# Kernel tuning notes

Measured on AMD Instinct MI355X. Metric: run time of the kernel, lower is better.

Reference implementation:

```python
import jax, jax.numpy as jnp
import numpy as np

DIM = 384
HEADS = 12
WS = 7
HID = 4 * 256  # FFN hidden is hard-coded default 1024, NOT 4*dim
EPS = 1e-5


def layernorm(x, g, b):
    mu = jnp.mean(x, axis=-1, keepdims=True)
    var = jnp.mean(jnp.square(x - mu), axis=-1, keepdims=True)
    return (x - mu) * jax.lax.rsqrt(var + EPS) * g + b


def setup_inputs() -> dict:
    key = jax.random.key(0)
    ks = jax.random.split(key, 12)
    s = 0.02
    return {
        "x": jax.random.normal(ks[0], (32, DIM, 56, 56), dtype=jnp.float32),
        "ln1_g": jnp.ones((DIM,), jnp.float32),
        "ln1_b": jnp.zeros((DIM,), jnp.float32),
        "qkv_w": jax.random.normal(ks[1], (3 * DIM, DIM), jnp.float32) * s,
        "qkv_b": jnp.zeros((3 * DIM,), jnp.float32),
        "proj_w": jax.random.normal(ks[2], (DIM, DIM), jnp.float32) * s,
        "proj_b": jnp.zeros((DIM,), jnp.float32),
        "ln2_g": jnp.ones((DIM,), jnp.float32),
        "ln2_b": jnp.zeros((DIM,), jnp.float32),
        "fc1_w": jax.random.normal(ks[3], (HID, DIM), jnp.float32) * s,
        "fc1_b": jnp.zeros((HID,), jnp.float32),
        "fc2_w": jax.random.normal(ks[4], (DIM, HID), jnp.float32) * s,
        "fc2_b": jnp.zeros((DIM,), jnp.float32),
    }


def window_attention(x, qkv_w, qkv_b, proj_w, proj_b):
    # x: [B, H, W, C] channels-last
    B, H, W, C = x.shape
    Wh, Ww = H // WS, W // WS
    # partition: [B*Wh*Ww, WS*WS, C]
    w = x.reshape(B, Wh, WS, Ww, WS, C).transpose(0, 1, 3, 2, 4, 5)
    w = w.reshape(B * Wh * Ww, WS * WS, C)
    Bn, N, _ = w.shape
    hd = C // HEADS
    qkv = w @ qkv_w.T + qkv_b  # [Bn, N, 3C]
    qkv = qkv.reshape(Bn, N, 3, HEADS, hd).transpose(2, 0, 3, 1, 4)
    q, k, v = qkv[0], qkv[1], qkv[2]  # each [Bn, h, N, hd]
    attn = jnp.einsum('bhnd,bhmd->bhnm', q, k) * (hd ** -0.5)
    attn = jax.nn.softmax(attn, axis=-1)
    o = jnp.einsum('bhnm,bhmd->bhnd', attn, v)
    o = o.transpose(0, 2, 1, 3).reshape(Bn, N, C)
    o = o @ proj_w.T + proj_b
    # reverse
    o = o.reshape(B, Wh, Ww, WS, WS, C).transpose(0, 1, 3, 2, 4, 5)
    return o.reshape(B, H, W, C)


def reference(x, ln1_g, ln1_b, qkv_w, qkv_b, proj_w, proj_b,
              ln2_g, ln2_b, fc1_w, fc1_b, fc2_w, fc2_b):
    # x: [B, C, H, W]
    residual = x
    h = x.transpose(0, 2, 3, 1)  # [B,H,W,C]
    h = layernorm(h, ln1_g, ln1_b)
    h = window_attention(h, qkv_w, qkv_b, proj_w, proj_b)
    x = h.transpose(0, 3, 1, 2) + residual
    residual = x
    h = x.transpose(0, 2, 3, 1)
    h = layernorm(h, ln2_g, ln2_b)
    h = jax.nn.gelu(h @ fc1_w.T + fc1_b, approximate=False)
    h = h @ fc2_w.T + fc2_b
    return h.transpose(0, 3, 1, 2) + residual
```

## Files before the change

### kernel.cpp

```cpp
#include <hip/hip_runtime.h>
#include <cstdint>
#include <cmath>

#define DIM 384
#define HEADS 12
#define TOKENS 100352
#define HW_ 3136
#define NWIN 2048

typedef __attribute__((ext_vector_type(8))) short short8;
typedef __attribute__((ext_vector_type(4))) short short4v;
typedef __attribute__((ext_vector_type(2))) short short2v;
typedef __attribute__((ext_vector_type(4))) float f32x4;

#define AS1 __attribute__((address_space(1)))
#define AS3 __attribute__((address_space(3)))

__device__ __forceinline__ short f2b(float f){
  unsigned u = __builtin_bit_cast(unsigned, f);
  u += 0x7FFFu + ((u >> 16) & 1u);
  return (short)(u >> 16);
}
__device__ __forceinline__ float b2f(short h){
  unsigned u = ((unsigned)(unsigned short)h) << 16;
  return __builtin_bit_cast(float, u);
}

__device__ __forceinline__ void gload_lds16(const short* g, short* l){
  __builtin_amdgcn_global_load_lds((AS1 void*)(g), (AS3 void*)(l), 16, 0, 0);
}

__device__ __forceinline__ float gelu_f(float v){
  float z  = v * 0.70710678118654752f;
  float az = fabsf(z);
  float t  = __builtin_amdgcn_rcpf(1.f + 0.3275911f*az);
  float poly = t*(0.254829592f + t*(-0.284496736f + t*(1.421413741f +
               t*(-1.453152027f + t*1.061405429f))));
  float e  = __expf(-z*z);
  float er = copysignf(1.f - poly*e, z);
  return 0.5f * v * (1.f + er);
}

__global__ void k_cvt(const float* __restrict__ s, short* __restrict__ d, int n){
  int i = blockIdx.x*256 + threadIdx.x;
  if (i < n) d[i] = f2b(s[i]);
}

__global__ __launch_bounds__(256) void k_ln1(const float* __restrict__ x,
    const float* __restrict__ gam, const float* __restrict__ bet,
    short* __restrict__ ln1, short* __restrict__ xr)
{
  __shared__ float red0[256];
  __shared__ float red1[256];
  __shared__ float mus[64], rss[64];
  __shared__ short lnc[64*36];
  __shared__ short xc[64*36];
  int t = threadIdx.x;
  int blk = blockIdx.x;
  int b = blk / 49;
  int hw0 = (blk % 49) * 64;
  int p = t & 63, cq = t >> 6;
  const float* xb = x + (long)b*DIM*HW_ + hw0 + p;
  float s = 0.f, sq = 0.f;
  for (int i = 0; i < 96; i++){
    int c = i*4 + cq;
    float v = xb[(long)c*HW_];
    s += v; sq += v*v;
  }
  red0[t] = s; red1[t] = sq;
  __syncthreads();
  if (t < 64){
    float ts = red0[t] + red0[t+64] + red0[t+128] + red0[t+192];
    float tq = red1[t] + red1[t+64] + red1[t+128] + red1[t+192];
    float mu = ts * (1.f/DIM);
    float var = tq * (1.f/DIM) - mu*mu;
    mus[t] = mu;
    rss[t] = rsqrtf(var + 1e-5f);
  }
  __syncthreads();
  float mu_p = mus[p], rs_p = rss[p];
  int p2 = t >> 2, q4 = t & 3;
  int hwp2 = hw0 + p2;
  int h2 = hwp2 / 56, w2 = hwp2 % 56;
  int wt2 = ((b*8 + h2/7)*8 + w2/7)*49 + (h2%7)*7 + (w2%7);
  long lnbase = (long)wt2*DIM;
  long xrbase = (long)(b*HW_ + hwp2)*DIM;
  for (int cc0 = 0; cc0 < DIM; cc0 += 32){
    #pragma unroll
    for (int u = 0; u < 8; u++){
      int c = cc0 + cq*8 + u;
      float v = xb[(long)c*HW_];
      float nv = (v - mu_p)*rs_p*gam[c] + bet[c];
      lnc[p*36 + cq*8 + u] = f2b(nv);
      xc[p*36 + cq*8 + u] = f2b(v);
    }
    __syncthreads();
    short8 av, bv;
    #pragma unroll
    for (int u = 0; u < 8; u++){
      av[u] = lnc[p2*36 + q4*8 + u];
      bv[u] = xc[p2*36 + q4*8 + u];
    }
    *(short8*)(ln1 + lnbase + cc0 + q4*8) = av;
    *(short8*)(xr + xrbase + cc0 + q4*8) = bv;
    __syncthreads();
  }
}

#define EPI_BIAS 0
#define EPI_PROJ 1
#define EPI_GELU 2
#define EPI_OUT  4

template<int EPI>
__global__ __launch_bounds__(256) void k_gemm(
    const short* __restrict__ A, const short* __restrict__ B,
    const float* __restrict__ bias, short* __restrict__ out,
    const short* __restrict__ res, int M, int N, int K, int ntiles)
{
  constexpr int ES  = (EPI == EPI_OUT) ? 133  : 132;
  constexpr int SMF = (EPI == EPI_OUT) ? 8512 : 8448;
  __shared__ float smemf[SMF];
  short* AsP = (short*)smemf;
  short* BsP = (short*)(smemf + 4096);
  float* E   = smemf;

  int nwg = gridDim.x;
  int orig = blockIdx.x;
  int bid = (orig & 7) * (nwg >> 3) + (orig >> 3);
  int nt = bid % ntiles, mt = bid / ntiles;
  int m0 = mt*128, n0 = nt*128;
  int t = threadIdx.x;
  int lane = t & 63, wv = t >> 6;
  int wm = wv >> 1, wn = wv & 1;
  int gg = lane >> 4, cc = lane & 15;

  int srow = t >> 2;
  int skc = ((t & 3) ^ (srow & 3)) << 3;
  const short* Ab = A + (long)(m0 + srow)*K + skc;
  const short* Bb = B + (long)(n0 + srow)*K + skc;
  long rowstep = 64L*K;

  int goff = (gg << 3) ^ ((cc & 3) << 3);

  f32x4 acc[4][4];
  #pragma unroll
  for (int i=0;i<4;i++)
    #pragma unroll
    for (int j=0;j<4;j++) acc[i][j] = (f32x4){0.f,0.f,0.f,0.f};

  gload_lds16(Ab,           AsP + t*8);
  gload_lds16(Ab + rowstep, AsP + (t+256)*8);
  gload_lds16(Bb,           BsP + t*8);
  gload_lds16(Bb + rowstep, BsP + (t+256)*8);

  int nk = K >> 5;
  for (int kt = 0; kt < nk; kt++){
    int cur = kt & 1;
    __syncthreads();
    if (kt + 1 < nk){
      int nxt = cur ^ 1;
      long ko = (long)(kt + 1) << 5;
      gload_lds16(Ab + ko,           AsP + nxt*4096 + t*8);
      gload_lds16(Ab + ko + rowstep, AsP + nxt*4096 + (t+256)*8);
      gload_lds16(Bb + ko,           BsP + nxt*4096 + t*8);
      gload_lds16(Bb + ko + rowstep, BsP + nxt*4096 + (t+256)*8);
    }
    const short* Ac = AsP + cur*4096;
    const short* Bc = BsP + cur*4096;
    short8 af[4], bfv[4];
    #pragma unroll
    for (int mi=0;mi<4;mi++) af[mi] = *(const short8*)(Ac + (wm*64 + mi*16 + cc)*32 + goff);
    #pragma unroll
    for (int ni=0;ni<4;ni++) bfv[ni] = *(const short8*)(Bc + (wn*64 + ni*16 + cc)*32 + goff);
    #pragma unroll
    for (int mi=0;mi<4;mi++)
      #pragma unroll
      for (int ni=0;ni<4;ni++)
        acc[mi][ni] = __builtin_amdgcn_mfma_f32_16x16x32_bf16(af[mi], bfv[ni], acc[mi][ni], 0, 0, 0);
  }

  if constexpr (EPI == EPI_OUT) {
    float* outf = (float*)out;
    #pragma unroll
    for (int p = 0; p < 2; p++){
      __syncthreads();
      if (wm == p){
        #pragma unroll
        for (int mi=0;mi<4;mi++){
          #pragma unroll
          for (int r=0;r<4;r++){
            float* Er = E + (mi*16 + gg*4 + r)*ES + wn*64 + cc;
            Er[0]  = acc[mi][0][r];
            Er[16] = acc[mi][1][r];
            Er[32] = acc[mi][2][r];
            Er[48] = acc[mi][3][r];
          }
        }
      }
      __syncthreads();
      #pragma unroll
      for (int jj = 0; jj < 8; jj++){
        int unit = jj*256 + t;
        int crow = unit >> 5, chunk = unit & 31;
        int row = m0 + p*64 + crow;
        f32x4 v = *(const f32x4*)(E + crow*ES + chunk*4);
        f32x4 bv = *(const f32x4*)(bias + n0 + chunk*4);
        short4v rv = *(const short4v*)(res + (long)row*N + n0 + chunk*4);
        #pragma unroll
        for (int j = 0; j < 4; j++) v[j] += bv[j] + b2f(rv[j]);
        *(f32x4*)(E + crow*ES + chunk*4) = v;
      }
      __syncthreads();
      #pragma unroll
      for (int jj = 0; jj < 32; jj++){
        int unit = jj*256 + t;
        int c = unit >> 6, rl = unit & 63;
        int token = m0 + p*64 + rl;
        int b = token / HW_;
        int hw = token - b*HW_;
        outf[((long)b*DIM + n0 + c)*HW_ + hw] = E[rl*ES + c];
      }
    }
  } else {
    #pragma unroll
    for (int p = 0; p < 2; p++){
      __syncthreads();
      #pragma unroll
      for (int mh = 0; mh < 2; mh++){
        #pragma unroll
        for (int r = 0; r < 4; r++){
          int crow = wm*32 + mh*16 + gg*4 + r;
          float* Er = E + crow*ES + wn*64 + cc;
          Er[0]  = acc[mh*2 + p][0][r];
          Er[16] = acc[mh*2 + p][1][r];
          Er[32] = acc[mh*2 + p][2][r];
          Er[48] = acc[mh*2 + p][3][r];
        }
      }
      __syncthreads();
      #pragma unroll
      for (int jj = 0; jj < 8; jj++){
        int unit = jj*256 + t;
        int crow = unit >> 5, chunk = unit & 31;
        int rr = crow & 15, mh = (crow >> 4) & 1, wmr = crow >> 5;
        int row = m0 + wmr*64 + (mh*2 + p)*16 + rr;
        int col = n0 + chunk*4;
        f32x4 v = *(const f32x4*)(E + crow*ES + chunk*4);
        f32x4 bv = *(const f32x4*)(bias + col);
        long orow;
        if constexpr (EPI == EPI_PROJ) {
          int b = row / HW_; int rem = row % HW_;
          int wid = rem / 49, idx = rem % 49;
          int hh = (wid >> 3)*7 + idx/7;
          int ww = (wid & 7)*7 + idx%7;
          orow = (long)(b*HW_ + hh*56 + ww)*N;
        } else {
          orow = (long)row*N;
        }
        float vv[4];
        #pragma unroll
        for (int j = 0; j < 4; j++){
          vv[j] = v[j] + bv[j];
          if constexpr (EPI == EPI_GELU) vv[j] = gelu_f(vv[j]);
        }
        if constexpr (EPI == EPI_PROJ){
          short4v rv = *(const short4v*)(res + orow + col);
          #pragma unroll
          for (int j = 0; j < 4; j++) vv[j] += b2f(rv[j]);
        }
        short4v ov;
        #pragma unroll
        for (int j = 0; j < 4; j++) ov[j] = f2b(vv[j]);
        *(short4v*)(out + orow + col) = ov;
      }
    }
  }
}

__global__ __launch_bounds__(256) void k_ln2(const short* __restrict__ x2,
  const float* __restrict__ gam, const float* __restrict__ bet, short* __restrict__ o)
{
  int t = threadIdx.x, lane = t & 63, wv = t >> 6;
  long row = (long)blockIdx.x*4 + wv;
  const short* xr = x2 + row*DIM;
  short4v a = *(const short4v*)(xr + lane*4);
  short2v b2 = *(const short2v*)(xr + 256 + lane*2);
  float f[6] = {b2f(a[0]),b2f(a[1]),b2f(a[2]),b2f(a[3]),b2f(b2[0]),b2f(b2[1])};
  float s = 0.f, sq = 0.f;
  #pragma unroll
  for (int i=0;i<6;i++){ s += f[i]; sq += f[i]*f[i]; }
  #pragma unroll
  for (int off=1; off<64; off<<=1){ s += __shfl_xor(s, off); sq += __shfl_xor(sq, off); }
  float mu = s*(1.f/DIM);
  float var = sq*(1.f/DIM) - mu*mu;
  float rs = rsqrtf(var + 1e-5f);
  int c0 = lane*4, c1 = 256 + lane*2;
  short4v oa; short2v ob;
  #pragma unroll
  for (int i=0;i<4;i++) oa[i] = f2b((f[i]-mu)*rs*gam[c0+i] + bet[c0+i]);
  #pragma unroll
  for (int j=0;j<2;j++) ob[j] = f2b((f[4+j]-mu)*rs*gam[c1+j] + bet[c1+j]);
  *(short4v*)(o + row*DIM + c0) = oa;
  *(short2v*)(o + row*DIM + c1) = ob;
}

__global__ __launch_bounds__(256) void k_attn(const short* __restrict__ qkv, short* __restrict__ o)
{
  __shared__ short lds[4*7424];
  int t = threadIdx.x;
  int lane = t & 63, wv = t >> 6;
  int w = blockIdx.x;
  short* Qs = lds + wv*7424;
  short* Ks = Qs + 2560;
  short* Vt = Ks + 2560;
  short* Pl = Qs;
  int g = lane >> 4, c = lane & 15;
  int nrow = lane >> 2;
  int dc = (lane & 3) * 8;
  const float scale = 0.17677669529663687f;
  for (int hh = 0; hh < 3; hh++){
    int h = wv + hh*4;
    __syncthreads();
    long base = (long)w*49*1152 + h*32;
    #pragma unroll
    for (int it = 0; it < 4; it++){
      int n = it*16 + nrow;
      short8 vq = {0,0,0,0,0,0,0,0};
      short8 vk = vq, vvv = vq;
      if (n < 49){
        vq  = *(const short8*)(qkv + base + (long)n*1152 + dc);
        vk  = *(const short8*)(qkv + base + (long)n*1152 + 384 + dc);
        vvv = *(const short8*)(qkv + base + (long)n*1152 + 768 + dc);
      }
      *(short8*)(Qs + n*40 + dc) = vq;
      *(short8*)(Ks + n*40 + dc) = vk;
      #pragma unroll
      for (int u = 0; u < 8; u++) Vt[(dc+u)*72 + n] = vvv[u];
    }
    __syncthreads();
    f32x4 sacc[4][4];
    #pragma unroll
    for (int i=0;i<4;i++)
      #pragma unroll
      for (int j=0;j<4;j++) sacc[i][j] = (f32x4){0.f,0.f,0.f,0.f};
    short8 kf[4];
    #pragma unroll
    for (int ni=0;ni<4;ni++) kf[ni] = *(const short8*)(Ks + (ni*16 + c)*40 + g*8);
    #pragma unroll
    for (int mi=0;mi<4;mi++){
      short8 a = *(const short8*)(Qs + (mi*16 + c)*40 + g*8);
      #pragma unroll
      for (int ni=0;ni<4;ni++)
        sacc[mi][ni] = __builtin_amdgcn_mfma_f32_16x16x32_bf16(a, kf[ni], sacc[mi][ni], 0, 0, 0);
    }
    #pragma unroll
    for (int mi=0;mi<4;mi++){
      #pragma unroll
      for (int r=0;r<4;r++){
        float v0 = sacc[mi][0][r]*scale;
        float v1 = sacc[mi][1][r]*scale;
        float v2 = sacc[mi][2][r]*scale;
        float v3 = (c >= 1) ? -1e30f : sacc[mi][3][r]*scale;
        float mx = fmaxf(fmaxf(v0,v1), fmaxf(v2,v3));
        #pragma unroll
        for (int off=1; off<16; off<<=1) mx = fmaxf(mx, __shfl_xor(mx, off));
        float e0 = __expf(v0-mx), e1 = __expf(v1-mx), e2 = __expf(v2-mx), e3 = __expf(v3-mx);
        float sm = e0+e1+e2+e3;
        #pragma unroll
        for (int off=1; off<16; off<<=1) sm += __shfl_xor(sm, off);
        float inv = 1.f/sm;
        int prow = mi*16 + g*4 + r;
        Pl[prow*72 +      c] = f2b(e0*inv);
        Pl[prow*72 + 16 + c] = f2b(e1*inv);
        Pl[prow*72 + 32 + c] = f2b(e2*inv);
        Pl[prow*72 + 48 + c] = f2b(e3*inv);
      }
    }
    __syncthreads();
    f32x4 oacc[4][2];
    #pragma unroll
    for (int i=0;i<4;i++){ oacc[i][0] = (f32x4){0.f,0.f,0.f,0.f}; oacc[i][1] = oacc[i][0]; }
    #pragma unroll
    for (int ks=0; ks<2; ks++){
      short8 bb0 = *(const short8*)(Vt + (c)*72      + ks*32 + g*8);
      short8 bb1 = *(const short8*)(Vt + (16 + c)*72 + ks*32 + g*8);
      #pragma unroll
      for (int mi=0;mi<4;mi++){
        short8 aa = *(const short8*)(Pl + (mi*16 + c)*72 + ks*32 + g*8);
        oacc[mi][0] = __builtin_amdgcn_mfma_f32_16x16x32_bf16(aa, bb0, oacc[mi][0], 0, 0, 0);
        oacc[mi][1] = __builtin_amdgcn_mfma_f32_16x16x32_bf16(aa, bb1, oacc[mi][1], 0, 0, 0);
      }
    }
    #pragma unroll
    for (int mi=0;mi<4;mi++){
      #pragma unroll
      for (int r=0;r<4;r++){
        int row = mi*16 + g*4 + r;
        if (row < 49){
          long ob = ((long)w*49 + row)*384 + h*32;
          o[ob + c]      = f2b(oacc[mi][0][r]);
          o[ob + 16 + c] = f2b(oacc[mi][1][r]);
        }
      }
    }
  }
}

extern "C" void kernel_launch(void* const* d_in, const int* in_sizes, int n_in,
                              void* d_out, int out_size, void* d_ws, size_t ws_size,
                              hipStream_t stream) {
  (void)in_sizes; (void)n_in; (void)out_size; (void)ws_size;
  const float* x      = (const float*)d_in[0];
  const float* ln1_g  = (const float*)d_in[1];
  const float* ln1_b  = (const float*)d_in[2];
  const float* qkv_w  = (const float*)d_in[3];
  const float* qkv_b  = (const float*)d_in[4];
  const float* proj_w = (const float*)d_in[5];
  const float* proj_b = (const float*)d_in[6];
  const float* ln2_g  = (const float*)d_in[7];
  const float* ln2_b  = (const float*)d_in[8];
  const float* fc1_w  = (const float*)d_in[9];
  const float* fc1_b  = (const float*)d_in[10];
  const float* fc2_w  = (const float*)d_in[11];
  const float* fc2_b  = (const float*)d_in[12];

  char* ws = (char*)d_ws;
  short* buf1 = (short*)(ws);
  short* buf2 = (short*)(ws + 231211008L);
  short* buf3 = (short*)(ws + 308281344L);
  short* buf4 = (short*)(ws + 385351680L);
  short* buf5 = (short*)(ws + 462422016L);
  short* wq = (short*)(ws + 539492352L);
  short* wp = wq + 442368;
  short* w1 = wp + 147456;
  short* w2 = w1 + 393216;

  k_cvt<<<dim3((442368+255)/256), dim3(256), 0, stream>>>(qkv_w, wq, 442368);
  k_cvt<<<dim3((147456+255)/256), dim3(256), 0, stream>>>(proj_w, wp, 147456);
  k_cvt<<<dim3((393216+255)/256), dim3(256), 0, stream>>>(fc1_w, w1, 393216);
  k_cvt<<<dim3((393216+255)/256), dim3(256), 0, stream>>>(fc2_w, w2, 393216);

  k_ln1<<<dim3(1568), dim3(256), 0, stream>>>(x, ln1_g, ln1_b, buf2, buf5);

  k_gemm<EPI_BIAS><<<dim3(784*9), dim3(256), 0, stream>>>(buf2, wq, qkv_b, buf1, nullptr,
                                                          TOKENS, 1152, 384, 9);
  k_attn<<<dim3(NWIN), dim3(256), 0, stream>>>(buf1, buf3);

  k_gemm<EPI_PROJ><<<dim3(784*3), dim3(256), 0, stream>>>(buf3, wp, proj_b, buf4, buf5,
                                                          TOKENS, 384, 384, 3);
  k_ln2<<<dim3(TOKENS/4), dim3(256), 0, stream>>>(buf4, ln2_g, ln2_b, buf2);

  k_gemm<EPI_GELU><<<dim3(784*8), dim3(256), 0, stream>>>(buf2, w1, fc1_b, buf1, nullptr,
                                                          TOKENS, 1024, 384, 8);
  k_gemm<EPI_OUT><<<dim3(784*3), dim3(256), 0, stream>>>(buf1, w2, fc2_b, (short*)d_out, buf4,
                                                         TOKENS, 384, 1024, 3);
}
```

Baseline: 766.4 us.

## Triple-buffer A tiles and use partial vmcnt waits in GEMM main loop

Restructures the GEMM k-loop so A tiles are prefetched two steps ahead in a three-slot LDS ring while B stays double-buffered. The full __syncthreads drain is replaced by an explicit s_waitcnt vmcnt(2) plus s_barrier, so the next A tile's global-to-LDS load can stay in flight across the barrier. The aim is to hide more global load latency behind MFMA work. In exchange LDS use grows to 40KB per block, which may lower occupancy, and the correctness of the vmcnt counting depends on the exact order in which loads are issued.

```diff
diff --git a/kernel.cpp b/kernel.cpp
--- a/kernel.cpp
+++ b/kernel.cpp
@@ -118,12 +118,9 @@
     const float* __restrict__ bias, short* __restrict__ out,
     const short* __restrict__ res, int M, int N, int K, int ntiles)
 {
-  constexpr int ES  = (EPI == EPI_OUT) ? 133  : 132;
-  constexpr int SMF = (EPI == EPI_OUT) ? 8512 : 8448;
-  __shared__ float smemf[SMF];
-  short* AsP = (short*)smemf;
-  short* BsP = (short*)(smemf + 4096);
-  float* E   = smemf;
+  constexpr int ES = (EPI == EPI_OUT) ? 133 : 132;
+  __shared__ short sm[20480];
+  float* E = (float*)sm;
 
   int nwg = gridDim.x;
   int orig = blockIdx.x;
@@ -149,25 +146,34 @@
     #pragma unroll
     for (int j=0;j<4;j++) acc[i][j] = (f32x4){0.f,0.f,0.f,0.f};
 
-  gload_lds16(Ab,           AsP + t*8);
-  gload_lds16(Ab + rowstep, AsP + (t+256)*8);
-  gload_lds16(Bb,           BsP + t*8);
-  gload_lds16(Bb + rowstep, BsP + (t+256)*8);
-
   int nk = K >> 5;
+
+  gload_lds16(Ab,           sm + t*8);
+  gload_lds16(Ab + rowstep, sm + (t+256)*8);
+  gload_lds16(Bb,           sm + 12288 + t*8);
+  gload_lds16(Bb + rowstep, sm + 12288 + (t+256)*8);
+  gload_lds16(Ab + 32,           sm + 4096 + t*8);
+  gload_lds16(Ab + 32 + rowstep, sm + 4096 + (t+256)*8);
+
+  int ac = 0, bc = 0;
   for (int kt = 0; kt < nk; kt++){
-    int cur = kt & 1;
-    __syncthreads();
+    if (kt + 1 < nk) { asm volatile("s_waitcnt vmcnt(2) lgkmcnt(0)" ::: "memory"); }
+    else             { asm volatile("s_waitcnt vmcnt(0) lgkmcnt(0)" ::: "memory"); }
+    __builtin_amdgcn_s_barrier();
     if (kt + 1 < nk){
-      int nxt = cur ^ 1;
-      long ko = (long)(kt + 1) << 5;
-      gload_lds16(Ab + ko,           AsP + nxt*4096 + t*8);
-      gload_lds16(Ab + ko + rowstep, AsP + nxt*4096 + (t+256)*8);
-      gload_lds16(Bb + ko,           BsP + nxt*4096 + t*8);
-      gload_lds16(Bb + ko + rowstep, BsP + nxt*4096 + (t+256)*8);
-    }
-    const short* Ac = AsP + cur*4096;
-    const short* Bc = BsP + cur*4096;
+      long ko = (long)(kt+1) << 5;
+      int bn = bc ^ 1;
+      gload_lds16(Bb + ko,           sm + 12288 + bn*4096 + t*8);
+      gload_lds16(Bb + ko + rowstep, sm + 12288 + bn*4096 + (t+256)*8);
+    }
+    if (kt + 2 < nk){
+      long ko = (long)(kt+2) << 5;
+      int an = ac + 2; if (an >= 3) an -= 3;
+      gload_lds16(Ab + ko,           sm + an*4096 + t*8);
+      gload_lds16(Ab + ko + rowstep, sm + an*4096 + (t+256)*8);
+    }
+    const short* Ac = sm + ac*4096;
+    const short* Bc = sm + 12288 + bc*4096;
     short8 af[4], bfv[4];
     #pragma unroll
     for (int mi=0;mi<4;mi++) af[mi] = *(const short8*)(Ac + (wm*64 + mi*16 + cc)*32 + goff);
@@ -178,6 +184,8 @@
       #pragma unroll
       for (int ni=0;ni<4;ni++)
         acc[mi][ni] = __builtin_amdgcn_mfma_f32_16x16x32_bf16(af[mi], bfv[ni], acc[mi][ni], 0, 0, 0);
+    ac = (ac + 1 == 3) ? 0 : ac + 1;
+    bc ^= 1;
   }
 
   if constexpr (EPI == EPI_OUT) {
```

Result: no change. 760.1 us (-0.8%).
